# Kernel tuning notes

Measured on AMD Instinct MI355X. Metric: run time of the kernel, lower is better.

The kernel has to match this reference:

```python
import jax, jax.numpy as jnp
import numpy as np

HEADS = 8
D_MODEL = 512
D_K = D_MODEL // HEADS


def setup_inputs() -> dict:
    key = jax.random.key(0)
    k1, k2, k3, k4 = jax.random.split(key, 4)
    N, S = 4, 2048
    queries = jax.random.normal(k1, (N, S, D_MODEL), dtype=jnp.float32)
    keys = jax.random.normal(k2, (N, S, D_MODEL), dtype=jnp.float32)
    values = jax.random.normal(k3, (N, S, D_MODEL), dtype=jnp.float32)
    W_out = jax.random.normal(k4, (D_MODEL, D_MODEL), dtype=jnp.float32) * (1.0 / np.sqrt(D_MODEL))
    b_out = jnp.zeros((D_MODEL,), dtype=jnp.float32)
    return {"queries": queries, "keys": keys, "values": values, "W_out": W_out, "b_out": b_out}


def reference(queries, keys, values, W_out, b_out):
    N, Q, _ = queries.shape
    K = keys.shape[1]
    # NOTE: the original module defines q/k/v Linear layers but never applies
    # them in forward; inputs are reshaped directly into heads.
    q = queries.reshape(N, Q, HEADS, D_K)
    k = keys.reshape(N, K, HEADS, D_K)
    v = values.reshape(N, K, HEADS, D_K)
    # energy: [N, H, Q, K] -- full score matrix materialized, as in source
    energy = jnp.einsum('nqhd,nkhd->nhqk', q, k)
    # Quirk preserved: scale by sqrt(d_model), not sqrt(d_k)
    attn_w = jax.nn.softmax(energy / np.sqrt(D_MODEL), axis=3)
    attention = jnp.einsum('nhql,nlhd->nqhd', attn_w, v).reshape(N, Q, D_MODEL)
    # fc_output: torch Linear computes x @ W.T + b
    out = attention @ W_out.T + b_out
    return out
```

## Files before the change

kernel.cpp:

```cpp
#include <hip/hip_runtime.h>
#include <hip/hip_bf16.h>
#include <cstdint>
#include <cstddef>

#define S_LEN 2048
#define DM 512
#define DK 64

typedef __attribute__((ext_vector_type(4))) float f32x4;
typedef __attribute__((ext_vector_type(8))) short short8;

__device__ __forceinline__ unsigned short f2bf(float f) {
  union { float f; uint32_t u; } c; c.f = f;
  uint32_t u = c.u;
  u += 0x7FFF + ((u >> 16) & 1);
  return (unsigned short)(u >> 16);
}

__device__ __forceinline__ unsigned int pkbf(float a, float b) {
  union { __hip_bfloat162 h; unsigned int u; } c;
  c.h = __float22bfloat162_rn(make_float2(a, b));
  return c.u;
}

__device__ __forceinline__ short8 ldq8(const float* p, float s) {
  float4 a = *reinterpret_cast<const float4*>(p);
  float4 b = *reinterpret_cast<const float4*>(p + 4);
  union { short8 v; unsigned int u[4]; } r;
  r.u[0] = pkbf(a.x * s, a.y * s);
  r.u[1] = pkbf(a.z * s, a.w * s);
  r.u[2] = pkbf(b.x * s, b.y * s);
  r.u[3] = pkbf(b.z * s, b.w * s);
  return r.v;
}

__device__ __forceinline__ void gl2lds16(const unsigned short* g, unsigned short* l) {
  __builtin_amdgcn_global_load_lds(
      (const __attribute__((address_space(1))) unsigned int*)g,
      (__attribute__((address_space(3))) unsigned int*)l, 16, 0, 0);
}

__global__ __launch_bounds__(256) void prep_kernel(const float* __restrict__ K,
                                                   const float* __restrict__ V,
                                                   const float* __restrict__ W,
                                                   unsigned short* __restrict__ Kb,
                                                   unsigned short* __restrict__ Vt,
                                                   unsigned short* __restrict__ Wb) {
  __shared__ unsigned short tile[64][66];
  const int bid = blockIdx.x;
  const int t = threadIdx.x;
  if (bid < 4096) {
    int i = (bid * 256 + t) * 4;
    float4 v = *reinterpret_cast<const float4*>(K + i);
    ushort4 o;
    o.x = f2bf(v.x); o.y = f2bf(v.y); o.z = f2bf(v.z); o.w = f2bf(v.w);
    *reinterpret_cast<ushort4*>(Kb + i) = o;
  } else if (bid < 4352) {
    int i = ((bid - 4096) * 256 + t) * 4;
    float4 v = *reinterpret_cast<const float4*>(W + i);
    ushort4 o;
    o.x = f2bf(v.x); o.y = f2bf(v.y); o.z = f2bf(v.z); o.w = f2bf(v.w);
    *reinterpret_cast<ushort4*>(Wb + i) = o;
  } else {
    const int r = bid - 4352;
    const int lt = r & 31;
    const int nh = r >> 5;
    const int n = nh >> 3, h = nh & 7;
    #pragma unroll
    for (int it = 0; it < 16; ++it) {
      int e = it * 256 + t;
      int l = e >> 6, d = e & 63;
      float v = V[((size_t)(n * S_LEN + lt * 64 + l)) * DM + h * DK + d];
      tile[l][d] = f2bf(v);
    }
    __syncthreads();
    #pragma unroll
    for (int it = 0; it < 16; ++it) {
      int e = it * 256 + t;
      int d = e >> 6, l = e & 63;
      Vt[((size_t)(nh * DK + d)) * S_LEN + lt * 64 + l] = tile[l][d];
    }
  }
}

__global__ __launch_bounds__(256, 2) void attn_kernel(const float* __restrict__ Qf,
                                                      const unsigned short* __restrict__ Kb,
                                                      const unsigned short* __restrict__ Vt,
                                                      unsigned short* __restrict__ Ab) {
  __shared__ __align__(16) unsigned short KT[2][64 * 64];
  __shared__ __align__(16) unsigned short VT[2][64 * 64];
  __shared__ __align__(16) unsigned short PL[4][32 * 64];

  const int dlin = blockIdx.x + 16 * blockIdx.y;
  const int xcd = dlin & 7;
  const int mm = dlin >> 3;
  const int nh = xcd * 4 + (mm & 3);
  const int qsb = mm >> 2;
  const int n = nh >> 3, h = nh & 7;
  const int wave = threadIdx.x >> 6;
  const int lane = threadIdx.x & 63;
  const int lr = lane & 15;
  const int lg = lane >> 4;
  const int r7 = lr & 7;

  const int q0 = qsb * 128 + wave * 32;
  const float C2 = 0.063758716f;

  short8 qa[2][2];
  #pragma unroll
  for (int f = 0; f < 2; ++f) {
    const float* qp = Qf + ((size_t)(n * S_LEN + q0 + f * 16 + lr)) * DM + h * DK + lg * 8;
    qa[f][0] = ldq8(qp, C2);
    qa[f][1] = ldq8(qp + 32, C2);
  }

  f32x4 oacc[2][4];
  #pragma unroll
  for (int f = 0; f < 2; ++f)
    #pragma unroll
    for (int dt = 0; dt < 4; ++dt) oacc[f][dt] = (f32x4){0.f, 0.f, 0.f, 0.f};
  float lsum[2] = {0.f, 0.f};

  const int srow = lane >> 3;
  const int csrc = (lane & 7) ^ srow;
  const unsigned short* ksrc = Kb + ((size_t)(n * S_LEN + srow)) * DM + h * DK + csrc * 8;
  const unsigned short* vsrc = Vt + ((size_t)(nh * DK + srow)) * S_LEN + csrc * 8;
  const int kr0 = wave * 16;

#define STAGE(B_, L0_) do {                                                        \
    _Pragma("unroll")                                                              \
    for (int u = 0; u < 2; ++u)                                                    \
      gl2lds16(ksrc + (size_t)((L0_) + kr0 + u * 8) * DM, &KT[B_][(kr0 + u * 8) * 64]); \
    _Pragma("unroll")                                                              \
    for (int u = 0; u < 2; ++u)                                                    \
      gl2lds16(vsrc + (size_t)(kr0 + u * 8) * S_LEN + (L0_), &VT[B_][(kr0 + u * 8) * 64]); \
  } while (0)

#define COMPUTE(B_) do {                                                           \
    f32x4 s[4][2];                                                                 \
    _Pragma("unroll")                                                              \
    for (int nt = 0; nt < 4; ++nt) {                                               \
      const short8 kb0 = *reinterpret_cast<const short8*>(                         \
          &KT[B_][(nt * 16 + lr) * 64 + ((lg ^ r7) << 3)]);                        \
      const short8 kb1 = *reinterpret_cast<const short8*>(                         \
          &KT[B_][(nt * 16 + lr) * 64 + (((4 + lg) ^ r7) << 3)]);                  \
      _Pragma("unroll")                                                            \
      for (int f = 0; f < 2; ++f) {                                                \
        s[nt][f] = (f32x4){0.f, 0.f, 0.f, 0.f};                                    \
        s[nt][f] = __builtin_amdgcn_mfma_f32_16x16x32_bf16(kb0, qa[f][0], s[nt][f], 0, 0, 0); \
        s[nt][f] = __builtin_amdgcn_mfma_f32_16x16x32_bf16(kb1, qa[f][1], s[nt][f], 0, 0, 0); \
      }                                                                            \
    }                                                                              \
    _Pragma("unroll")                                                              \
    for (int nt = 0; nt < 4; ++nt)                                                 \
      _Pragma("unroll")                                                            \
      for (int f = 0; f < 2; ++f) {                                                \
        float p0 = __builtin_amdgcn_exp2f(s[nt][f][0]);                            \
        float p1 = __builtin_amdgcn_exp2f(s[nt][f][1]);                            \
        float p2 = __builtin_amdgcn_exp2f(s[nt][f][2]);                            \
        float p3 = __builtin_amdgcn_exp2f(s[nt][f][3]);                            \
        lsum[f] += (p0 + p1) + (p2 + p3);                                          \
        uint2 w; w.x = pkbf(p0, p1); w.y = pkbf(p2, p3);                           \
        *reinterpret_cast<uint2*>(&PL[wave][(f * 16 + lr) * 64 +                   \
            (((nt * 2 + (lg >> 1)) ^ r7) << 3) + ((lg & 1) << 2)]) = w;            \
      }                                                                            \
    _Pragma("unroll")                                                              \
    for (int kc = 0; kc < 2; ++kc) {                                               \
      const int prc = ((kc * 4 + lg) ^ r7) << 3;                                   \
      const short8 pa0 = *reinterpret_cast<const short8*>(&PL[wave][lr * 64 + prc]); \
      const short8 pa1 = *reinterpret_cast<const short8*>(&PL[wave][(16 + lr) * 64 + prc]); \
      _Pragma("unroll")                                                            \
      for (int dt = 0; dt < 4; ++dt) {                                             \
        const short8 vb = *reinterpret_cast<const short8*>(                        \
            &VT[B_][(dt * 16 + lr) * 64 + prc]);                                   \
        oacc[0][dt] = __builtin_amdgcn_mfma_f32_16x16x32_bf16(pa0, vb, oacc[0][dt], 0, 0, 0); \
        oacc[1][dt] = __builtin_amdgcn_mfma_f32_16x16x32_bf16(pa1, vb, oacc[1][dt], 0, 0, 0); \
      }                                                                            \
    }                                                                              \
  } while (0)

  STAGE(0, 0);
  asm volatile("s_waitcnt vmcnt(0)" ::: "memory");
  __syncthreads();

  for (int l0 = 0; l0 < S_LEN; l0 += 64) {
    const int cur = (l0 >> 6) & 1;
    if (l0 + 64 < S_LEN) STAGE(cur ^ 1, l0 + 64);
    COMPUTE(cur);
    __syncthreads();
  }
#undef STAGE
#undef COMPUTE

  #pragma unroll
  for (int f = 0; f < 2; ++f) {
    lsum[f] += __shfl_xor(lsum[f], 16);
    lsum[f] += __shfl_xor(lsum[f], 32);
  }

  unsigned short* ab = Ab + ((size_t)(n * S_LEN + q0)) * DM + h * DK + lr;
  #pragma unroll
  for (int f = 0; f < 2; ++f)
    #pragma unroll
    for (int j = 0; j < 4; ++j) {
      float rl = 1.f / __shfl(lsum[f], lg * 4 + j);
      #pragma unroll
      for (int dt = 0; dt < 4; ++dt)
        ab[(size_t)(f * 16 + lg * 4 + j) * DM + dt * 16] = f2bf(oacc[f][dt][j] * rl);
    }
}

__global__ __launch_bounds__(256, 2) void proj_kernel(const unsigned short* __restrict__ Ab,
                                                      const unsigned short* __restrict__ Wb,
                                                      const float* __restrict__ bias,
                                                      float* __restrict__ out) {
  __shared__ __align__(16) unsigned short At[2][128 * 64];
  __shared__ __align__(16) unsigned short Wt[2][64 * 64];

  const int m0 = blockIdx.x * 128;
  const int o0 = blockIdx.y * 64;
  const int wave = threadIdx.x >> 6;
  const int lane = threadIdx.x & 63;
  const int lr = lane & 15;
  const int lg = lane >> 4;
  const int r7 = lr & 7;
  const int wm = (wave >> 1) * 64;
  const int wn = (wave & 1) * 32;

  const int srow = lane >> 3;
  const int csrc = (lane & 7) ^ srow;
  const unsigned short* asrc = Ab + ((size_t)(m0 + wave * 32 + srow)) * DM + csrc * 8;
  const unsigned short* wsrc = Wb + ((size_t)(o0 + wave * 16 + srow)) * DM + csrc * 8;

  float bv[2];
  #pragma unroll
  for (int nf = 0; nf < 2; ++nf) bv[nf] = bias[o0 + wn + nf * 16 + lr];

  f32x4 acc[4][2];
  #pragma unroll
  for (int mf = 0; mf < 4; ++mf)
    #pragma unroll
    for (int nf = 0; nf < 2; ++nf) acc[mf][nf] = (f32x4){0.f, 0.f, 0.f, 0.f};

#define PSTAGE(B_, KB_) do {                                                       \
    _Pragma("unroll")                                                              \
    for (int u = 0; u < 4; ++u)                                                    \
      gl2lds16(asrc + (size_t)(u * 8) * DM + (KB_), &At[B_][(wave * 32 + u * 8) * 64]); \
    _Pragma("unroll")                                                              \
    for (int u = 0; u < 2; ++u)                                                    \
      gl2lds16(wsrc + (size_t)(u * 8) * DM + (KB_), &Wt[B_][(wave * 16 + u * 8) * 64]); \
  } while (0)

#define PCOMPUTE(B_) do {                                                          \
    _Pragma("unroll")                                                              \
    for (int kc = 0; kc < 2; ++kc) {                                               \
      const int sw = ((kc * 4 + lg) ^ r7) << 3;                                    \
      short8 af[4], wf[2];                                                         \
      _Pragma("unroll")                                                            \
      for (int mf = 0; mf < 4; ++mf)                                               \
        af[mf] = *reinterpret_cast<const short8*>(&At[B_][(wm + mf * 16 + lr) * 64 + sw]); \
      _Pragma("unroll")                                                            \
      for (int nf = 0; nf < 2; ++nf)                                               \
        wf[nf] = *reinterpret_cast<const short8*>(&Wt[B_][(wn + nf * 16 + lr) * 64 + sw]); \
      _Pragma("unroll")                                                            \
      for (int mf = 0; mf < 4; ++mf)                                               \
        _Pragma("unroll")                                                          \
        for (int nf = 0; nf < 2; ++nf)                                             \
          acc[mf][nf] = __builtin_amdgcn_mfma_f32_16x16x32_bf16(af[mf], wf[nf], acc[mf][nf], 0, 0, 0); \
    }                                                                              \
  } while (0)

  PSTAGE(0, 0);
  asm volatile("s_waitcnt vmcnt(0)" ::: "memory");
  __syncthreads();

  for (int kb = 0; kb < DM; kb += 64) {
    const int cur = (kb >> 6) & 1;
    if (kb + 64 < DM) PSTAGE(cur ^ 1, kb + 64);
    PCOMPUTE(cur);
    __syncthreads();
  }
#undef PSTAGE
#undef PCOMPUTE

  #pragma unroll
  for (int mf = 0; mf < 4; ++mf) {
    #pragma unroll
    for (int j = 0; j < 4; ++j) {
      float* op = out + (size_t)(m0 + wm + mf * 16 + lg * 4 + j) * DM + o0 + wn + lr;
      #pragma unroll
      for (int nf = 0; nf < 2; ++nf)
        op[nf * 16] = acc[mf][nf][j] + bv[nf];
    }
  }
}

extern "C" void kernel_launch(void* const* d_in, const int* in_sizes, int n_in,
                              void* d_out, int out_size, void* d_ws, size_t ws_size,
                              hipStream_t stream) {
  const float* Q = (const float*)d_in[0];
  const float* K = (const float*)d_in[1];
  const float* V = (const float*)d_in[2];
  const float* W = (const float*)d_in[3];
  const float* b = (const float*)d_in[4];
  float* out = (float*)d_out;

  char* ws = (char*)d_ws;
  unsigned short* Kb = (unsigned short*)(ws);
  unsigned short* Vt = (unsigned short*)(ws + 8388608);
  unsigned short* Ab = (unsigned short*)(ws + 16777216);
  unsigned short* Wb = (unsigned short*)(ws + 25165824);

  prep_kernel<<<5376, 256, 0, stream>>>(K, V, W, Kb, Vt, Wb);
  attn_kernel<<<dim3(16, 32), 256, 0, stream>>>(Q, Kb, Vt, Ab);
  proj_kernel<<<dim3(64, 8), 256, 0, stream>>>(Ab, Wb, b, out);
}
```

Measured before the change: 73.08 us.

## Keep softmax probabilities in registers via fp16 MFMA and split keys across waves

The attention kernel now feeds the exp'd scores straight from registers into a 16x16x16 fp16 MFMA for P·V. This removes the per-wave LDS round trip for P, and V is stored as fp16 to match. Each block handles 64 queries with two waves per query group, each covering half the keys. The partial outputs and row sums are combined through LDS at the end. The grid doubles, and the launch-bounds target rises to four blocks per CU to improve occupancy. The cost is a final cross-wave reduction, a smaller per-block query tile (so K/V tiles are reloaded more often per query), and fp16 precision for P and V.

```diff
diff --git a/kernel.cpp b/kernel.cpp
--- a/kernel.cpp
+++ b/kernel.cpp
@@ -9,12 +9,17 @@
 
 typedef __attribute__((ext_vector_type(4))) float f32x4;
 typedef __attribute__((ext_vector_type(8))) short short8;
+typedef __attribute__((ext_vector_type(4))) _Float16 f16x4;
 
 __device__ __forceinline__ unsigned short f2bf(float f) {
   union { float f; uint32_t u; } c; c.f = f;
   uint32_t u = c.u;
   u += 0x7FFF + ((u >> 16) & 1);
   return (unsigned short)(u >> 16);
+}
+
+__device__ __forceinline__ unsigned short f2h(float f) {
+  union { _Float16 h; unsigned short u; } c; c.h = (_Float16)f; return c.u;
 }
 
 __device__ __forceinline__ unsigned int pkbf(float a, float b) {
@@ -71,7 +76,7 @@
       int e = it * 256 + t;
       int l = e >> 6, d = e & 63;
       float v = V[((size_t)(n * S_LEN + lt * 64 + l)) * DM + h * DK + d];
-      tile[l][d] = f2bf(v);
+      tile[l][d] = f2h(v);
     }
     __syncthreads();
     #pragma unroll
@@ -83,42 +88,44 @@
   }
 }
 
-__global__ __launch_bounds__(256, 2) void attn_kernel(const float* __restrict__ Qf,
+__global__ __launch_bounds__(256, 4) void attn_kernel(const float* __restrict__ Qf,
                                                       const unsigned short* __restrict__ Kb,
                                                       const unsigned short* __restrict__ Vt,
                                                       unsigned short* __restrict__ Ab) {
   __shared__ __align__(16) unsigned short KT[2][64 * 64];
   __shared__ __align__(16) unsigned short VT[2][64 * 64];
-  __shared__ __align__(16) unsigned short PL[4][32 * 64];
-
-  const int dlin = blockIdx.x + 16 * blockIdx.y;
+  __shared__ float lsL[2][2][16];
+
+  const int dlin = blockIdx.x + 32 * blockIdx.y;
   const int xcd = dlin & 7;
   const int mm = dlin >> 3;
   const int nh = xcd * 4 + (mm & 3);
-  const int qsb = mm >> 2;
+  const int qtb = mm >> 2;
   const int n = nh >> 3, h = nh & 7;
   const int wave = threadIdx.x >> 6;
   const int lane = threadIdx.x & 63;
-  const int lr = lane & 15;
-  const int lg = lane >> 4;
-  const int r7 = lr & 7;
-
-  const int q0 = qsb * 128 + wave * 32;
+  const int c = lane & 15;
+  const int g = lane >> 4;
+  const int qw = wave >> 1;
+  const int kw = wave & 1;
+  const int c7 = c & 7;
+
+  const int qbase = qtb * 64 + qw * 32;
   const float C2 = 0.063758716f;
 
-  short8 qa[2][2];
-  #pragma unroll
-  for (int f = 0; f < 2; ++f) {
-    const float* qp = Qf + ((size_t)(n * S_LEN + q0 + f * 16 + lr)) * DM + h * DK + lg * 8;
-    qa[f][0] = ldq8(qp, C2);
-    qa[f][1] = ldq8(qp + 32, C2);
-  }
+  short8 qfrag[2][2];
+  #pragma unroll
+  for (int qt = 0; qt < 2; ++qt)
+    #pragma unroll
+    for (int dkc = 0; dkc < 2; ++dkc)
+      qfrag[qt][dkc] = ldq8(
+          Qf + ((size_t)(n * S_LEN + qbase + qt * 16 + c)) * DM + h * DK + dkc * 32 + g * 8, C2);
 
   f32x4 oacc[2][4];
   #pragma unroll
-  for (int f = 0; f < 2; ++f)
-    #pragma unroll
-    for (int dt = 0; dt < 4; ++dt) oacc[f][dt] = (f32x4){0.f, 0.f, 0.f, 0.f};
+  for (int qt = 0; qt < 2; ++qt)
+    #pragma unroll
+    for (int dt = 0; dt < 4; ++dt) oacc[qt][dt] = (f32x4){0.f, 0.f, 0.f, 0.f};
   float lsum[2] = {0.f, 0.f};
 
   const int srow = lane >> 3;
@@ -137,46 +144,52 @@
   } while (0)
 
 #define COMPUTE(B_) do {                                                           \
-    f32x4 s[4][2];                                                                 \
-    _Pragma("unroll")                                                              \
-    for (int nt = 0; nt < 4; ++nt) {                                               \
-      const short8 kb0 = *reinterpret_cast<const short8*>(                         \
-          &KT[B_][(nt * 16 + lr) * 64 + ((lg ^ r7) << 3)]);                        \
-      const short8 kb1 = *reinterpret_cast<const short8*>(                         \
-          &KT[B_][(nt * 16 + lr) * 64 + (((4 + lg) ^ r7) << 3)]);                  \
-      _Pragma("unroll")                                                            \
-      for (int f = 0; f < 2; ++f) {                                                \
-        s[nt][f] = (f32x4){0.f, 0.f, 0.f, 0.f};                                    \
-        s[nt][f] = __builtin_amdgcn_mfma_f32_16x16x32_bf16(kb0, qa[f][0], s[nt][f], 0, 0, 0); \
-        s[nt][f] = __builtin_amdgcn_mfma_f32_16x16x32_bf16(kb1, qa[f][1], s[nt][f], 0, 0, 0); \
+    short8 kf[2][2];                                                               \
+    _Pragma("unroll")                                                              \
+    for (int ks = 0; ks < 2; ++ks)                                                 \
+      _Pragma("unroll")                                                            \
+      for (int dkc = 0; dkc < 2; ++dkc)                                            \
+        kf[ks][dkc] = *reinterpret_cast<const short8*>(                            \
+            &KT[B_][(kw * 32 + ks * 16 + c) * 64 + (((dkc * 4 + g) ^ c7) << 3)]);  \
+    f32x4 s[2][2];                                                                 \
+    _Pragma("unroll")                                                              \
+    for (int qt = 0; qt < 2; ++qt)                                                 \
+      _Pragma("unroll")                                                            \
+      for (int ks = 0; ks < 2; ++ks) s[qt][ks] = (f32x4){0.f, 0.f, 0.f, 0.f};      \
+    _Pragma("unroll")                                                              \
+    for (int dkc = 0; dkc < 2; ++dkc)                                              \
+      _Pragma("unroll")                                                            \
+      for (int ks = 0; ks < 2; ++ks)                                               \
+        _Pragma("unroll")                                                          \
+        for (int qt = 0; qt < 2; ++qt)                                             \
+          s[qt][ks] = __builtin_amdgcn_mfma_f32_16x16x32_bf16(                     \
+              kf[ks][dkc], qfrag[qt][dkc], s[qt][ks], 0, 0, 0);                    \
+    f16x4 pf[2][2];                                                                \
+    _Pragma("unroll")                                                              \
+    for (int qt = 0; qt < 2; ++qt)                                                 \
+      _Pragma("unroll")                                                            \
+      for (int ks = 0; ks < 2; ++ks) {                                             \
+        float p0 = __builtin_amdgcn_exp2f(s[qt][ks][0]);                           \
+        float p1 = __builtin_amdgcn_exp2f(s[qt][ks][1]);                           \
+        float p2 = __builtin_amdgcn_exp2f(s[qt][ks][2]);                           \
+        float p3 = __builtin_amdgcn_exp2f(s[qt][ks][3]);                           \
+        lsum[qt] += (p0 + p1) + (p2 + p3);                                         \
+        f16x4 pv; pv[0] = (_Float16)p0; pv[1] = (_Float16)p1;                      \
+        pv[2] = (_Float16)p2; pv[3] = (_Float16)p3;                                \
+        pf[qt][ks] = pv;                                                           \
       }                                                                            \
-    }                                                                              \
-    _Pragma("unroll")                                                              \
-    for (int nt = 0; nt < 4; ++nt)                                                 \
-      _Pragma("unroll")                                                            \
-      for (int f = 0; f < 2; ++f) {                                                \
-        float p0 = __builtin_amdgcn_exp2f(s[nt][f][0]);                            \
-        float p1 = __builtin_amdgcn_exp2f(s[nt][f][1]);                            \
-        float p2 = __builtin_amdgcn_exp2f(s[nt][f][2]);                            \
-        float p3 = __builtin_amdgcn_exp2f(s[nt][f][3]);                            \
-        lsum[f] += (p0 + p1) + (p2 + p3);                                          \
-        uint2 w; w.x = pkbf(p0, p1); w.y = pkbf(p2, p3);                           \
-        *reinterpret_cast<uint2*>(&PL[wave][(f * 16 + lr) * 64 +                   \
-            (((nt * 2 + (lg >> 1)) ^ r7) << 3) + ((lg & 1) << 2)]) = w;            \
+    _Pragma("unroll")                                                              \
+    for (int ks = 0; ks < 2; ++ks)                                                 \
+      _Pragma("unroll")                                                            \
+      for (int dt = 0; dt < 4; ++dt) {                                             \
+        const f16x4 vf = *reinterpret_cast<const f16x4*>(                          \
+            &VT[B_][(dt * 16 + c) * 64 +                                           \
+                ((((kw * 4 + ks * 2 + (g >> 1)) ^ c7) << 3) + ((g & 1) << 2))]);   \
+        _Pragma("unroll")                                                          \
+        for (int qt = 0; qt < 2; ++qt)                                             \
+          oacc[qt][dt] = __builtin_amdgcn_mfma_f32_16x16x16f16(                    \
+              vf, pf[qt][ks], oacc[qt][dt], 0, 0, 0);                              \
       }                                                                            \
-    _Pragma("unroll")                                                              \
-    for (int kc = 0; kc < 2; ++kc) {                                               \
-      const int prc = ((kc * 4 + lg) ^ r7) << 3;                                   \
-      const short8 pa0 = *reinterpret_cast<const short8*>(&PL[wave][lr * 64 + prc]); \
-      const short8 pa1 = *reinterpret_cast<const short8*>(&PL[wave][(16 + lr) * 64 + prc]); \
-      _Pragma("unroll")                                                            \
-      for (int dt = 0; dt < 4; ++dt) {                                             \
-        const short8 vb = *reinterpret_cast<const short8*>(                        \
-            &VT[B_][(dt * 16 + lr) * 64 + prc]);                                   \
-        oacc[0][dt] = __builtin_amdgcn_mfma_f32_16x16x32_bf16(pa0, vb, oacc[0][dt], 0, 0, 0); \
-        oacc[1][dt] = __builtin_amdgcn_mfma_f32_16x16x32_bf16(pa1, vb, oacc[1][dt], 0, 0, 0); \
-      }                                                                            \
-    }                                                                              \
   } while (0)
 
   STAGE(0, 0);
@@ -193,21 +206,39 @@
 #undef COMPUTE
 
   #pragma unroll
-  for (int f = 0; f < 2; ++f) {
-    lsum[f] += __shfl_xor(lsum[f], 16);
-    lsum[f] += __shfl_xor(lsum[f], 32);
-  }
-
-  unsigned short* ab = Ab + ((size_t)(n * S_LEN + q0)) * DM + h * DK + lr;
-  #pragma unroll
-  for (int f = 0; f < 2; ++f)
-    #pragma unroll
-    for (int j = 0; j < 4; ++j) {
-      float rl = 1.f / __shfl(lsum[f], lg * 4 + j);
+  for (int qt = 0; qt < 2; ++qt) {
+    lsum[qt] += __shfl_xor(lsum[qt], 16);
+    lsum[qt] += __shfl_xor(lsum[qt], 32);
+  }
+
+  float* red = reinterpret_cast<float*>(&KT[0][0]);
+  if (kw == 1) {
+    #pragma unroll
+    for (int qt = 0; qt < 2; ++qt)
       #pragma unroll
       for (int dt = 0; dt < 4; ++dt)
-        ab[(size_t)(f * 16 + lg * 4 + j) * DM + dt * 16] = f2bf(oacc[f][dt][j] * rl);
+        *reinterpret_cast<f32x4*>(red + (((qw * 2 + qt) * 4 + dt) << 8) + lane * 4) = oacc[qt][dt];
+    if (lane < 16) { lsL[qw][0][lane] = lsum[0]; lsL[qw][1][lane] = lsum[1]; }
+  }
+  __syncthreads();
+  if (kw == 0) {
+    #pragma unroll
+    for (int qt = 0; qt < 2; ++qt) {
+      #pragma unroll
+      for (int dt = 0; dt < 4; ++dt)
+        oacc[qt][dt] += *reinterpret_cast<const f32x4*>(
+            red + (((qw * 2 + qt) * 4 + dt) << 8) + lane * 4);
+      const float rl = 1.f / (lsum[qt] + lsL[qw][qt][c]);
+      unsigned short* ab = Ab + ((size_t)(n * S_LEN + qbase + qt * 16 + c)) * DM + h * DK;
+      #pragma unroll
+      for (int dt = 0; dt < 4; ++dt) {
+        uint2 w;
+        w.x = pkbf(oacc[qt][dt][0] * rl, oacc[qt][dt][1] * rl);
+        w.y = pkbf(oacc[qt][dt][2] * rl, oacc[qt][dt][3] * rl);
+        *reinterpret_cast<uint2*>(ab + dt * 16 + g * 4) = w;
+      }
     }
+  }
 }
 
 __global__ __launch_bounds__(256, 2) void proj_kernel(const unsigned short* __restrict__ Ab,
@@ -312,6 +343,6 @@
   unsigned short* Wb = (unsigned short*)(ws + 25165824);
 
   prep_kernel<<<5376, 256, 0, stream>>>(K, V, W, Kb, Vt, Wb);
-  attn_kernel<<<dim3(16, 32), 256, 0, stream>>>(Q, Kb, Vt, Ab);
+  attn_kernel<<<dim3(32, 32), 256, 0, stream>>>(Q, Kb, Vt, Ab);
   proj_kernel<<<dim3(64, 8), 256, 0, stream>>>(Ab, Wb, b, out);
 }
```

Measured after the change: 75.55 us. +3.4%, slower.
